# Kernel optimization log

Hardware: AMD Instinct MI355X
Metric: run time of the kernel (lower is better)

The kernel has to match this reference:

```python
import jax, jax.numpy as jnp
import numpy as np

B, D1, D2, D3 = 4, 64, 64, 64
CIN, COUT = 32, 32
M1, M2, M3 = 8, 8, 8


def setup_inputs() -> dict:
    key = jax.random.key(0)
    k1, k2, k3 = jax.random.split(key, 3)
    x = jax.random.normal(k1, (B, D1, D2, D3, CIN), dtype=jnp.float32)
    # scale ~ random_normal initializer (stddev 0.05 default in keras)
    w_real = jax.random.normal(k2, (CIN, COUT, M1, M2, M3), dtype=jnp.float32) * 0.05
    w_imag = jax.random.normal(k3, (CIN, COUT, M1, M2, M3), dtype=jnp.float32) * 0.05
    return {"x": x, "w_real": w_real, "w_imag": w_imag}


def reference(x, w_real, w_imag):
    # tf.signal.fft3d transforms the innermost 3 dims of [B,D1,D2,D3,C]
    x_ft = jnp.fft.fftn(x.astype(jnp.complex64), axes=(2, 3, 4))
    # low-mode truncation over axes 1,2,3 (as in the original code)
    x_low = x_ft[:, :M1, :M2, :M3, :]                       # [B,M1,M2,M3,CIN]
    w = (w_real + 1j * w_imag).astype(jnp.complex64)         # [CIN,COUT,M1,M2,M3]
    x_low = jnp.transpose(x_low, (0, 4, 1, 2, 3))            # [B,CIN,M1,M2,M3]
    # Faithful to original: i,j of weights are summed out, k is matched.
    out_low = jnp.einsum('bcmnk,coijk->bomnk', x_low, w)     # [B,COUT,M1,M2,M3]
    out_low = jnp.transpose(out_low, (0, 2, 3, 4, 1))        # [B,M1,M2,M3,COUT]
    # zero-padded spectrum (replaces the wasteful tensor_scatter_nd_update)
    out_ft = jnp.zeros((B, D1, D2, D3, COUT), dtype=jnp.complex64)
    out_ft = out_ft.at[:, :M1, :M2, :M3, :].set(out_low)
    y = jnp.fft.ifftn(out_ft, axes=(2, 3, 4))
    return jnp.real(y).astype(jnp.float32)
```

## Files before the change

kernel.cpp:

```cpp
#include <hip/hip_runtime.h>


#define PI2F 6.28318530717958647692f

typedef float vf4 __attribute__((ext_vector_type(4)));

__global__ void k_weff(const float* __restrict__ wr, const float* __restrict__ wi,
                       float2* __restrict__ Weff) {
    __shared__ float2 ls[256];
    int t = threadIdx.x;
    int eL = t & 31, ijg = t >> 5;
    int e = blockIdx.x * 32 + eL;
    int base = (e >> 3) * 512 + (e & 7) + ijg * 64;
    float sr = 0.f, si = 0.f;
    #pragma unroll
    for (int j = 0; j < 8; ++j) { sr += wr[base + j * 8]; si += wi[base + j * 8]; }
    ls[t] = make_float2(sr, si);
    __syncthreads();
    if (t < 32) {
        float2 a = ls[t];
        #pragma unroll
        for (int g = 1; g < 8; ++g) { float2 v = ls[g * 32 + t]; a.x += v.x; a.y += v.y; }
        Weff[blockIdx.x * 32 + t] = a;
    }
}

__global__ void k_T(const float2* __restrict__ Weff, float2* __restrict__ T) {
    __shared__ float2 tw32[32];
    __shared__ float2 P[1024];
    __shared__ float2 A[256];
    int t = threadIdx.x;
    int c = blockIdx.x;
    if (t < 32) {
        float s, co_;
        __sincosf((PI2F / 32.f) * (float)t, &s, &co_);
        tw32[t] = make_float2(co_, s);
    }
    __syncthreads();
    {
        int g = t >> 8, rem = t & 255;
        float2 acc = make_float2(0.f, 0.f);
        #pragma unroll
        for (int k = 0; k < 8; ++k) {
            int fc = g * 8 + k;
            float2 v = Weff[fc * 256 + rem];
            float2 e = tw32[(fc * c) & 31];
            acc.x += v.x * e.x + v.y * e.y;
            acc.y += v.y * e.x - v.x * e.y;
        }
        P[t] = acc;
    }
    __syncthreads();
    if (t < 256) {
        float2 a = P[t];
        #pragma unroll
        for (int g = 1; g < 4; ++g) { float2 v = P[g * 256 + t]; a.x += v.x; a.y += v.y; }
        A[t] = a;
    }
    __syncthreads();
    {
        int g = t >> 8, rem = t & 255;
        int f3 = rem >> 5, co = rem & 31;
        float2 acc = make_float2(0.f, 0.f);
        #pragma unroll
        for (int k = 0; k < 8; ++k) {
            int o = g * 8 + k;
            float2 v = A[o * 8 + f3];
            float2 e = tw32[(o * co) & 31];
            acc.x += v.x * e.x - v.y * e.y;
            acc.y += v.x * e.y + v.y * e.x;
        }
        P[t] = acc;
    }
    __syncthreads();
    if (t < 256) {
        float2 a = P[t];
        #pragma unroll
        for (int g = 1; g < 4; ++g) { float2 v = P[g * 256 + t]; a.x += v.x; a.y += v.y; }
        T[c * 256 + t] = a;
    }
}

__global__ void k_dft2(const float* __restrict__ x, float2* __restrict__ S1) {
    __shared__ float2 tw64[64];
    __shared__ float2 P[2048];
    int t = threadIdx.x;
    int gid = blockIdx.x;
    int d3 = gid & 63, s = gid >> 6;
    int b = s >> 3, d1 = s & 7;
    int c = t & 31, d2g = t >> 5;
    if (t < 64) {
        float sn, cs;
        __sincosf((PI2F / 64.f) * (float)t, &sn, &cs);
        tw64[t] = make_float2(cs, sn);
    }
    __syncthreads();
    const float* xp = x + (size_t)b * 8388608 + (size_t)d1 * 131072 + d3 * 32 + c;
    float2 acc[8];
    #pragma unroll
    for (int f2 = 0; f2 < 8; ++f2) acc[f2] = make_float2(0.f, 0.f);
    #pragma unroll
    for (int k = 0; k < 8; ++k) {
        int d2 = d2g * 8 + k;
        float v = xp[d2 * 2048];
        #pragma unroll
        for (int f2 = 0; f2 < 8; ++f2) {
            float2 e = tw64[(f2 * d2) & 63];
            acc[f2].x += v * e.x;
            acc[f2].y -= v * e.y;
        }
    }
    #pragma unroll
    for (int f2 = 0; f2 < 8; ++f2) P[(d2g * 8 + f2) * 32 + c] = acc[f2];
    __syncthreads();
    {
        int f2 = t >> 5, cc = t & 31;
        float2 a = make_float2(0.f, 0.f);
        #pragma unroll
        for (int g = 0; g < 8; ++g) {
            float2 v = P[(g * 8 + f2) * 32 + cc];
            a.x += v.x; a.y += v.y;
        }
        S1[(size_t)(s * 8 + f2) * 2048 + d3 * 32 + cc] = a;
    }
}

__global__ void k_mix(const float2* __restrict__ S1, const float2* __restrict__ T,
                      float2* __restrict__ s5g) {
    __shared__ float2 sl1[2048];
    __shared__ float2 P[1024];
    __shared__ float2 s2[256];
    __shared__ float2 tw[64];
    int t = threadIdx.x;
    int gid = blockIdx.x;
    if (t < 64) {
        float sn, cs;
        __sincosf((PI2F / 64.f) * (float)t, &sn, &cs);
        tw[t] = make_float2(cs, sn);
    }
    {
        const float4* src = (const float4*)(S1 + (size_t)gid * 2048);
        ((float4*)sl1)[t] = src[t];
    }
    __syncthreads();
    {
        int g = t >> 8, rem = t & 255;
        int f3 = rem >> 5, c = rem & 31;
        float2 a = make_float2(0.f, 0.f);
        #pragma unroll 4
        for (int k = 0; k < 16; ++k) {
            int d3 = g * 16 + k;
            float2 v = sl1[d3 * 32 + c];
            float2 e = tw[(f3 * d3) & 63];
            a.x += v.x * e.x + v.y * e.y;
            a.y += v.y * e.x - v.x * e.y;
        }
        P[t] = a;
    }
    __syncthreads();
    if (t < 256) {
        float2 a = P[t];
        #pragma unroll
        for (int g = 1; g < 4; ++g) { float2 v = P[g * 256 + t]; a.x += v.x; a.y += v.y; }
        s2[t] = a;
    }
    __syncthreads();
    {
        int g = t >> 8, rem = t & 255;
        int f3 = rem >> 5, co = rem & 31;
        float2 a = make_float2(0.f, 0.f);
        #pragma unroll
        for (int k = 0; k < 8; ++k) {
            int cc = g * 8 + k;
            float2 v = s2[f3 * 32 + cc];
            float2 w = T[cc * 256 + f3 * 32 + co];
            a.x += v.x * w.x - v.y * w.y;
            a.y += v.x * w.y + v.y * w.x;
        }
        P[t] = a;
    }
    __syncthreads();
    if (t < 256) {
        float2 a = P[t];
        #pragma unroll
        for (int g = 1; g < 4; ++g) { float2 v = P[g * 256 + t]; a.x += v.x; a.y += v.y; }
        s5g[(size_t)gid * 256 + t] = a;
    }
}

__global__ void k_final3(const float2* __restrict__ s5g, float* __restrict__ out) {
    __shared__ float2 ls5[2048];
    __shared__ float2 sq6[2048];
    __shared__ float2 tw[64];
    int t = threadIdx.x;
    int gid = blockIdx.x;
    int blk = gid & 7;
    int d1  = (gid >> 3) & 63;
    int b   = gid >> 9;
    int co4 = t & 7;
    int d3r8 = (t >> 3) & 7;
    int d2q = t >> 6;
    float* obase = out + (size_t)b * 8388608 + (size_t)d1 * 131072
                 + (blk * 8 + d3r8) * 32 + co4 * 4;
    if (d1 >= 8) {
        vf4 z = {0.f, 0.f, 0.f, 0.f};
        #pragma unroll
        for (int i = 0; i < 16; ++i) {
            int d2 = d2q * 16 + i;
            __builtin_nontemporal_store(z, (vf4*)(obase + d2 * 2048));
        }
        return;
    }
    if (t < 64) {
        float sn, cs;
        __sincosf((PI2F / 64.f) * (float)t, &sn, &cs);
        tw[t] = make_float2(cs, sn);
    }
    {
        const float4* src = (const float4*)(s5g + (size_t)(b * 8 + d1) * 2048);
        float4* dst = (float4*)ls5;
        #pragma unroll
        for (int j = 0; j < 4; ++j) dst[t + j * 256] = src[t + j * 256];
    }
    __syncthreads();
    {
        int co = t & 31, d3r = t >> 5;
        int d3 = blk * 8 + d3r;
        #pragma unroll
        for (int f2 = 0; f2 < 8; ++f2) {
            float2 a = make_float2(0.f, 0.f);
            #pragma unroll
            for (int f3 = 0; f3 < 8; ++f3) {
                float2 v = ls5[f2 * 256 + f3 * 32 + co];
                float2 e = tw[(f3 * d3) & 63];
                a.x += v.x * e.x - v.y * e.y;
                a.y += v.x * e.y + v.y * e.x;
            }
            sq6[f2 * 256 + d3r * 32 + co] = a;
        }
    }
    __syncthreads();
    float2 v[8][4];
    #pragma unroll
    for (int f2 = 0; f2 < 8; ++f2) {
        #pragma unroll
        for (int k = 0; k < 4; ++k)
            v[f2][k] = sq6[f2 * 256 + d3r8 * 32 + co4 * 4 + k];
    }
    const float sc = 1.f / 131072.f;
    #pragma unroll 2
    for (int i = 0; i < 16; ++i) {
        int d2 = d2q * 16 + i;
        float rx = 0.f, ry = 0.f, rz = 0.f, rw = 0.f;
        #pragma unroll
        for (int f2 = 0; f2 < 8; ++f2) {
            float2 e = tw[(f2 * d2) & 63];
            rx += v[f2][0].x * e.x - v[f2][0].y * e.y;
            ry += v[f2][1].x * e.x - v[f2][1].y * e.y;
            rz += v[f2][2].x * e.x - v[f2][2].y * e.y;
            rw += v[f2][3].x * e.x - v[f2][3].y * e.y;
        }
        vf4 r = {rx * sc, ry * sc, rz * sc, rw * sc};
        __builtin_nontemporal_store(r, (vf4*)(obase + d2 * 2048));
    }
}

extern "C" void kernel_launch(void* const* d_in, const int* in_sizes, int n_in,
                              void* d_out, int out_size, void* d_ws, size_t ws_size,
                              hipStream_t stream) {
    const float* x  = (const float*)d_in[0];
    const float* wr = (const float*)d_in[1];
    const float* wi = (const float*)d_in[2];
    float* out = (float*)d_out;

    float2* Weff = (float2*)d_ws;
    float2* T    = Weff + 8192;
    float2* S1   = T + 8192;
    float2* s5g  = S1 + 524288;

    k_weff  <<<256,  256,  0, stream>>>(wr, wi, Weff);
    k_T     <<<32,   1024, 0, stream>>>(Weff, T);
    k_dft2  <<<2048, 256,  0, stream>>>(x, S1);
    k_mix   <<<256,  1024, 0, stream>>>(S1, T, s5g);
    k_final3<<<2048, 256,  0, stream>>>(s5g, out);
}
```

Before: 222.6 us.

## Fuse weight reduction and output zero-fill into DFT kernel, shrink final grid

Moves the zero-filling of the d1>=8 output region and the Weff weight reduction into the first DFT kernel, so one launch covers them. The weight work runs in the 256 trailing blocks and the zero fill in the first 1792. The final kernel now launches only the 256 blocks that produce nonzero output. This removes one kernel launch and overlaps the large zero-store traffic with the input DFT's reads. In exchange the first kernel gets heavier and needs more shared memory per block.

```diff
diff --git a/kernel.cpp b/kernel.cpp
--- a/kernel.cpp
+++ b/kernel.cpp
@@ -5,85 +5,13 @@
 
 typedef float vf4 __attribute__((ext_vector_type(4)));
 
-__global__ void k_weff(const float* __restrict__ wr, const float* __restrict__ wi,
-                       float2* __restrict__ Weff) {
-    __shared__ float2 ls[256];
-    int t = threadIdx.x;
-    int eL = t & 31, ijg = t >> 5;
-    int e = blockIdx.x * 32 + eL;
-    int base = (e >> 3) * 512 + (e & 7) + ijg * 64;
-    float sr = 0.f, si = 0.f;
-    #pragma unroll
-    for (int j = 0; j < 8; ++j) { sr += wr[base + j * 8]; si += wi[base + j * 8]; }
-    ls[t] = make_float2(sr, si);
-    __syncthreads();
-    if (t < 32) {
-        float2 a = ls[t];
-        #pragma unroll
-        for (int g = 1; g < 8; ++g) { float2 v = ls[g * 32 + t]; a.x += v.x; a.y += v.y; }
-        Weff[blockIdx.x * 32 + t] = a;
-    }
-}
-
-__global__ void k_T(const float2* __restrict__ Weff, float2* __restrict__ T) {
-    __shared__ float2 tw32[32];
-    __shared__ float2 P[1024];
-    __shared__ float2 A[256];
-    int t = threadIdx.x;
-    int c = blockIdx.x;
-    if (t < 32) {
-        float s, co_;
-        __sincosf((PI2F / 32.f) * (float)t, &s, &co_);
-        tw32[t] = make_float2(co_, s);
-    }
-    __syncthreads();
-    {
-        int g = t >> 8, rem = t & 255;
-        float2 acc = make_float2(0.f, 0.f);
-        #pragma unroll
-        for (int k = 0; k < 8; ++k) {
-            int fc = g * 8 + k;
-            float2 v = Weff[fc * 256 + rem];
-            float2 e = tw32[(fc * c) & 31];
-            acc.x += v.x * e.x + v.y * e.y;
-            acc.y += v.y * e.x - v.x * e.y;
-        }
-        P[t] = acc;
-    }
-    __syncthreads();
-    if (t < 256) {
-        float2 a = P[t];
-        #pragma unroll
-        for (int g = 1; g < 4; ++g) { float2 v = P[g * 256 + t]; a.x += v.x; a.y += v.y; }
-        A[t] = a;
-    }
-    __syncthreads();
-    {
-        int g = t >> 8, rem = t & 255;
-        int f3 = rem >> 5, co = rem & 31;
-        float2 acc = make_float2(0.f, 0.f);
-        #pragma unroll
-        for (int k = 0; k < 8; ++k) {
-            int o = g * 8 + k;
-            float2 v = A[o * 8 + f3];
-            float2 e = tw32[(o * co) & 31];
-            acc.x += v.x * e.x - v.y * e.y;
-            acc.y += v.x * e.y + v.y * e.x;
-        }
-        P[t] = acc;
-    }
-    __syncthreads();
-    if (t < 256) {
-        float2 a = P[t];
-        #pragma unroll
-        for (int g = 1; g < 4; ++g) { float2 v = P[g * 256 + t]; a.x += v.x; a.y += v.y; }
-        T[c * 256 + t] = a;
-    }
-}
-
-__global__ void k_dft2(const float* __restrict__ x, float2* __restrict__ S1) {
+__global__ void k_dft2z(const float* __restrict__ x,
+                        const float* __restrict__ wr, const float* __restrict__ wi,
+                        float2* __restrict__ Weff, float2* __restrict__ S1,
+                        float* __restrict__ out) {
     __shared__ float2 tw64[64];
     __shared__ float2 P[2048];
+    __shared__ float2 ls[256];
     int t = threadIdx.x;
     int gid = blockIdx.x;
     int d3 = gid & 63, s = gid >> 6;
@@ -122,6 +50,88 @@
             a.x += v.x; a.y += v.y;
         }
         S1[(size_t)(s * 8 + f2) * 2048 + d3 * 32 + cc] = a;
+    }
+    if (gid < 1792) {
+        int pair = gid >> 3, sub = gid & 7;
+        int bb = pair / 56;
+        int dd1 = 8 + (pair - bb * 56);
+        float* zb = out + (size_t)bb * 8388608 + (size_t)dd1 * 131072 + sub * 16384;
+        vf4* zp = (vf4*)zb;
+        vf4 z = {0.f, 0.f, 0.f, 0.f};
+        #pragma unroll
+        for (int i = 0; i < 16; ++i)
+            __builtin_nontemporal_store(z, zp + i * 256 + t);
+    } else {
+        int eL = t & 31, ijg = t >> 5;
+        int e = (gid - 1792) * 32 + eL;
+        int base = (e >> 3) * 512 + (e & 7) + ijg * 64;
+        float sr = 0.f, si = 0.f;
+        #pragma unroll
+        for (int j = 0; j < 8; ++j) { sr += wr[base + j * 8]; si += wi[base + j * 8]; }
+        ls[t] = make_float2(sr, si);
+        __syncthreads();
+        if (t < 32) {
+            float2 a = ls[t];
+            #pragma unroll
+            for (int g = 1; g < 8; ++g) { float2 v = ls[g * 32 + t]; a.x += v.x; a.y += v.y; }
+            Weff[(gid - 1792) * 32 + t] = a;
+        }
+    }
+}
+
+__global__ void k_T(const float2* __restrict__ Weff, float2* __restrict__ T) {
+    __shared__ float2 tw32[32];
+    __shared__ float2 P[1024];
+    __shared__ float2 A[256];
+    int t = threadIdx.x;
+    int c = blockIdx.x;
+    if (t < 32) {
+        float s, co_;
+        __sincosf((PI2F / 32.f) * (float)t, &s, &co_);
+        tw32[t] = make_float2(co_, s);
+    }
+    __syncthreads();
+    {
+        int g = t >> 8, rem = t & 255;
+        float2 acc = make_float2(0.f, 0.f);
+        #pragma unroll
+        for (int k = 0; k < 8; ++k) {
+            int fc = g * 8 + k;
+            float2 v = Weff[fc * 256 + rem];
+            float2 e = tw32[(fc * c) & 31];
+            acc.x += v.x * e.x + v.y * e.y;
+            acc.y += v.y * e.x - v.x * e.y;
+        }
+        P[t] = acc;
+    }
+    __syncthreads();
+    if (t < 256) {
+        float2 a = P[t];
+        #pragma unroll
+        for (int g = 1; g < 4; ++g) { float2 v = P[g * 256 + t]; a.x += v.x; a.y += v.y; }
+        A[t] = a;
+    }
+    __syncthreads();
+    {
+        int g = t >> 8, rem = t & 255;
+        int f3 = rem >> 5, co = rem & 31;
+        float2 acc = make_float2(0.f, 0.f);
+        #pragma unroll
+        for (int k = 0; k < 8; ++k) {
+            int o = g * 8 + k;
+            float2 v = A[o * 8 + f3];
+            float2 e = tw32[(o * co) & 31];
+            acc.x += v.x * e.x - v.y * e.y;
+            acc.y += v.x * e.y + v.y * e.x;
+        }
+        P[t] = acc;
+    }
+    __syncthreads();
+    if (t < 256) {
+        float2 a = P[t];
+        #pragma unroll
+        for (int g = 1; g < 4; ++g) { float2 v = P[g * 256 + t]; a.x += v.x; a.y += v.y; }
+        T[c * 256 + t] = a;
     }
 }
 
@@ -188,36 +198,27 @@
     }
 }
 
-__global__ void k_final3(const float2* __restrict__ s5g, float* __restrict__ out) {
+__global__ void k_final3c(const float2* __restrict__ s5g, float* __restrict__ out) {
     __shared__ float2 ls5[2048];
     __shared__ float2 sq6[2048];
     __shared__ float2 tw[64];
     int t = threadIdx.x;
     int gid = blockIdx.x;
     int blk = gid & 7;
-    int d1  = (gid >> 3) & 63;
-    int b   = gid >> 9;
+    int s   = gid >> 3;
+    int b   = s >> 3, d1 = s & 7;
     int co4 = t & 7;
     int d3r8 = (t >> 3) & 7;
     int d2q = t >> 6;
     float* obase = out + (size_t)b * 8388608 + (size_t)d1 * 131072
                  + (blk * 8 + d3r8) * 32 + co4 * 4;
-    if (d1 >= 8) {
-        vf4 z = {0.f, 0.f, 0.f, 0.f};
-        #pragma unroll
-        for (int i = 0; i < 16; ++i) {
-            int d2 = d2q * 16 + i;
-            __builtin_nontemporal_store(z, (vf4*)(obase + d2 * 2048));
-        }
-        return;
-    }
     if (t < 64) {
         float sn, cs;
         __sincosf((PI2F / 64.f) * (float)t, &sn, &cs);
         tw[t] = make_float2(cs, sn);
     }
     {
-        const float4* src = (const float4*)(s5g + (size_t)(b * 8 + d1) * 2048);
+        const float4* src = (const float4*)(s5g + (size_t)s * 2048);
         float4* dst = (float4*)ls5;
         #pragma unroll
         for (int j = 0; j < 4; ++j) dst[t + j * 256] = src[t + j * 256];
@@ -278,9 +279,8 @@
     float2* S1   = T + 8192;
     float2* s5g  = S1 + 524288;
 
-    k_weff  <<<256,  256,  0, stream>>>(wr, wi, Weff);
-    k_T     <<<32,   1024, 0, stream>>>(Weff, T);
-    k_dft2  <<<2048, 256,  0, stream>>>(x, S1);
-    k_mix   <<<256,  1024, 0, stream>>>(S1, T, s5g);
-    k_final3<<<2048, 256,  0, stream>>>(s5g, out);
-}
+    k_dft2z  <<<2048, 256,  0, stream>>>(x, wr, wi, Weff, S1, out);
+    k_T      <<<32,   1024, 0, stream>>>(Weff, T);
+    k_mix    <<<256,  1024, 0, stream>>>(S1, T, s5g);
+    k_final3c<<<256,  256,  0, stream>>>(s5g, out);
+}
```

Result: no change. 224.0 us (+0.6%).
